# Optimization experiments

Hardware: AMD Instinct MI355X
Metric: run time of the kernel (lower is better)

## Reference

```python
import jax, jax.numpy as jnp
import numpy as np

N = 100000
H = 128
F_IN = 32
F_OUT = 16
NUM_GRAPHS = 64
NEG_SLOPE = 0.2


def setup_inputs() -> dict:
    key = jax.random.key(0)
    ks = jax.random.split(key, 16)
    inp = {
        'x': jax.random.normal(ks[0], (N, F_IN), dtype=jnp.float32),
        'edge_index': jax.random.randint(ks[1], (2, 1000000), 0, N, dtype=jnp.int32),
        'subgraph_edge_index': jax.random.randint(ks[2], (2, 1000000), 0, N, dtype=jnp.int32),
        'node_subnode_index': jax.random.randint(ks[3], (2, 200000), 0, N, dtype=jnp.int32),
        'subnode_node_index': jax.random.randint(ks[4], (2, 200000), 0, N, dtype=jnp.int32),
        'ground_node': jnp.arange(40000, dtype=jnp.int32),
        'subgraph_batch_index': jax.random.randint(ks[5], (60000,), 0, NUM_GRAPHS, dtype=jnp.int32),
        'batch_idx': jax.random.randint(ks[6], (40000,), 0, NUM_GRAPHS, dtype=jnp.int32),
    }
    s_in = 1.0 / np.sqrt(F_IN)
    s_h = 1.0 / np.sqrt(H)
    inp['emb_W'] = jax.random.uniform(ks[7], (F_IN, H), jnp.float32, -s_in, s_in)
    inp['emb_b'] = jax.random.uniform(ks[8], (H,), jnp.float32, -s_in, s_in)
    # 4 GATv2 layers (depth=1): lin_l, lin_r, att, bias per layer
    inp['Wl'] = jax.random.uniform(ks[9], (4, H, H), jnp.float32, -s_h, s_h)
    inp['Wr'] = jax.random.uniform(ks[10], (4, H, H), jnp.float32, -s_h, s_h)
    inp['att'] = jax.random.uniform(ks[11], (4, H), jnp.float32, -s_h, s_h)
    inp['bias'] = jax.random.uniform(ks[12], (4, H), jnp.float32, -s_h, s_h)
    inp['out_W'] = jax.random.uniform(ks[13], (H, F_OUT), jnp.float32, -s_h, s_h)
    inp['out_b'] = jax.random.uniform(ks[14], (F_OUT,), jnp.float32, -s_h, s_h)
    return inp


def _gatv2(x, ei, Wl, Wr, att, b):
    # add self loops (PyG GATv2Conv default add_self_loops=True)
    loops = jnp.broadcast_to(jnp.arange(N, dtype=ei.dtype)[None, :], (2, N))
    ei = jnp.concatenate([ei, loops], axis=1)
    src, dst = ei[0], ei[1]
    xl = x @ Wl  # source transform [N,H]
    xr = x @ Wr  # target transform [N,H]
    e = jax.nn.leaky_relu(xl[src] + xr[dst], NEG_SLOPE) @ att  # [E]
    m = jax.ops.segment_max(e, dst, num_segments=N)
    p = jnp.exp(e - m[dst])
    s = jax.ops.segment_sum(p, dst, num_segments=N)
    alpha = p / s[dst]
    out = jax.ops.segment_sum(alpha[:, None] * xl[src], dst, num_segments=N)
    return out + b


def reference(x, edge_index, subgraph_edge_index, node_subnode_index,
              subnode_node_index, ground_node, subgraph_batch_index, batch_idx,
              emb_W, emb_b, Wl, Wr, att, bias, out_W, out_b):
    h = x @ emb_W + emb_b
    eis = (edge_index, node_subnode_index, subgraph_edge_index, subnode_node_index)
    for i, ei in enumerate(eis):
        h = _gatv2(h, ei, Wl[i], Wr[i], att[i], bias[i])
    # global_add_pool over ground nodes
    pooled = jax.ops.segment_sum(h[ground_node], batch_idx, num_segments=NUM_GRAPHS)
    return pooled @ out_W + out_b
```

## Files before the change

kernel.cpp:

```cpp
#include <hip/hip_runtime.h>
#include <cstddef>


typedef __attribute__((ext_vector_type(8))) short bf16x8;
typedef __attribute__((ext_vector_type(4))) float f32x4;

#define NSH   10
#define CHUNK 8192
#define POOLP 256

__device__ __forceinline__ unsigned short f2bf(float f) {
  unsigned int u = __float_as_uint(f);
  u += 0x7fffu + ((u >> 16) & 1u);
  return (unsigned short)(u >> 16);
}
__device__ __forceinline__ unsigned short f2bf_rtz(float f) {
  return (unsigned short)(__float_as_uint(f) >> 16);
}
__device__ __forceinline__ float bf2f(short s) {
  return __uint_as_float(((unsigned int)(unsigned short)s) << 16);
}
__device__ __forceinline__ float2 unpk(unsigned int u) {
  return make_float2(__uint_as_float(u << 16),
                     __uint_as_float(u & 0xFFFF0000u));
}

__device__ __forceinline__ int lds_excl_scan(int* a, int len, int* aux, int tid)
{
  int g = (len + 255) >> 8;
  int lo = tid * g;
  int s = 0;
  for (int i = 0; i < g; ++i) { int idx = lo + i; if (idx < len) s += a[idx]; }
  aux[tid] = s;
  __syncthreads();
  for (int d = 1; d < 256; d <<= 1) {
    int v = (tid >= d) ? aux[tid - d] : 0;
    __syncthreads();
    aux[tid] += v;
    __syncthreads();
  }
  int run = aux[tid] - s;
  for (int i = 0; i < g; ++i) {
    int idx = lo + i;
    if (idx < len) { int t = a[idx]; a[idx] = run; run += t; }
  }
  int total = aux[255];
  __syncthreads();
  return total;
}

__device__ __forceinline__ void resolve_item(
    int id, int t1, int t2, int t3, int t4, int n,
    const int* s0, const int* s1, const int* s2, const int* s3,
    const int* d0, const int* d1, const int* d2, const int* d3,
    int& l, int& s, int& d, bool need_src)
{
  if (id < t4) {
    const int *sp, *dp; int e;
    if      (id < t1) { l = 0; e = id;      sp = s0; dp = d0; }
    else if (id < t2) { l = 1; e = id - t1; sp = s1; dp = d1; }
    else if (id < t3) { l = 2; e = id - t2; sp = s2; dp = d2; }
    else              { l = 3; e = id - t3; sp = s3; dp = d3; }
    d = dp[e];
    s = need_src ? sp[e] : 0;
  } else {
    int k = id - t4;
    l = (k >= 3 * n) ? 3 : (k >= 2 * n) ? 2 : (k >= n) ? 1 : 0;
    s = k - l * n; d = s;
  }
}

__global__ __launch_bounds__(256) void setup_kernel(
    const float* __restrict__ Wl, const float* __restrict__ Wr,
    const float* __restrict__ embW,
    unsigned short* __restrict__ packB, unsigned short* __restrict__ packE,
    int* __restrict__ offs4, int n, int e0, int e1, int e2, int e3)
{
  int id = blockIdx.x * 256 + threadIdx.x;
  if (id < 131072) {
    int j    = id & 7;
    int lane = (id >> 3) & 63;
    int kt   = (id >> 9) & 3;
    int ct   = (id >> 11) & 15;
    int l    = id >> 15;
    int k    = kt * 32 + (lane >> 4) * 8 + j;
    int col  = ct * 16 + (lane & 15);
    float v = (ct < 8) ? Wl[(size_t)l * 16384 + k * 128 + col]
                       : Wr[(size_t)l * 16384 + k * 128 + (col - 128)];
    packB[id] = f2bf(v);
  }
  int pe = id - 131072;
  if (pe >= 0 && pe < 4096) {
    int j    = pe & 7;
    int lane = (pe >> 3) & 63;
    int ct   = pe >> 9;
    int k    = (lane >> 4) * 8 + j;
    int col  = ct * 16 + (lane & 15);
    packE[pe] = f2bf(embW[k * 128 + col]);
  }
  int q = pe - 4096;
  if (q >= 0 && q < 4) {
    int El = (q == 0) ? e0 : (q == 1) ? e1 : (q == 2) ? e2 : e3;
    offs4[(size_t)q * (n + 1) + n] = El + n;
  }
}

__global__ __launch_bounds__(256) void embed_mfma_kernel(
    const float* __restrict__ x, const unsigned short* __restrict__ packE,
    const float* __restrict__ b, unsigned short* __restrict__ hb, int n)
{
  const int wave = threadIdx.x >> 6;
  const int lane = threadIdx.x & 63;
  const int rlan = lane & 15;
  const int kgrp = lane >> 4;

  bf16x8 Bf[8];
#pragma unroll
  for (int ct = 0; ct < 8; ++ct)
    Bf[ct] = *(const bf16x8*)(packE + ((size_t)ct * 64 + lane) * 8);
  float bv[8];
#pragma unroll
  for (int ct = 0; ct < 8; ++ct) bv[ct] = b[ct * 16 + rlan];

  const float4* __restrict__ x4 = (const float4*)x;
  const int ntiles = (n + 15) / 16;
  for (int tile = blockIdx.x * 4 + wave; tile < ntiles; tile += gridDim.x * 4) {
    int r = tile * 16 + rlan;
    if (r >= n) r = n - 1;
    float4 a0 = x4[(size_t)r * 8 + kgrp * 2];
    float4 a1 = x4[(size_t)r * 8 + kgrp * 2 + 1];
    bf16x8 Af;
    Af[0] = (short)f2bf(a0.x); Af[1] = (short)f2bf(a0.y);
    Af[2] = (short)f2bf(a0.z); Af[3] = (short)f2bf(a0.w);
    Af[4] = (short)f2bf(a1.x); Af[5] = (short)f2bf(a1.y);
    Af[6] = (short)f2bf(a1.z); Af[7] = (short)f2bf(a1.w);

    f32x4 acc[8];
#pragma unroll
    for (int ct = 0; ct < 8; ++ct) {
      acc[ct] = (f32x4){0.f, 0.f, 0.f, 0.f};
      acc[ct] = __builtin_amdgcn_mfma_f32_16x16x32_bf16(Af, Bf[ct], acc[ct], 0, 0, 0);
    }
    int rowb = tile * 16 + kgrp * 4;
#pragma unroll
    for (int ct = 0; ct < 8; ++ct) {
      int col = ct * 16 + rlan;
#pragma unroll
      for (int rr = 0; rr < 4; ++rr)
        if (rowb + rr < n)
          hb[(size_t)(rowb + rr) * 128 + col] = f2bf(acc[ct][rr] + bv[ct]);
    }
  }
}

__global__ __launch_bounds__(256) void gemm_mfma_kernel(
    const unsigned short* __restrict__ hb,
    const unsigned short* __restrict__ packB,
    unsigned short* __restrict__ xlb, unsigned short* __restrict__ xrb, int n)
{
  const int wave = threadIdx.x >> 6;
  const int lane = threadIdx.x & 63;
  const int rlan = lane & 15;
  const int kgrp = lane >> 4;

  bf16x8 Bf[4][4];
#pragma unroll
  for (int ct = 0; ct < 4; ++ct)
#pragma unroll
    for (int kt = 0; kt < 4; ++kt)
      Bf[ct][kt] = *(const bf16x8*)(packB +
          ((((size_t)(wave * 4 + ct)) * 4 + kt) * 64 + lane) * 8);

  unsigned short* __restrict__ outp = (wave < 2) ? xlb : xrb;
  const int colbase = (wave & 1) * 64;

  const int ntiles = (n + 31) / 32;
  for (int tile = blockIdx.x; tile < ntiles; tile += gridDim.x) {
    const int row0 = tile * 32;
    bf16x8 Af[2][4];
#pragma unroll
    for (int rt = 0; rt < 2; ++rt) {
      int r = row0 + rt * 16 + rlan;
      if (r >= n) r = n - 1;
      const unsigned short* ap = hb + (size_t)r * 128 + kgrp * 8;
#pragma unroll
      for (int kt = 0; kt < 4; ++kt)
        Af[rt][kt] = *(const bf16x8*)(ap + kt * 32);
    }
    f32x4 acc[2][4];
#pragma unroll
    for (int rt = 0; rt < 2; ++rt)
#pragma unroll
      for (int ct = 0; ct < 4; ++ct)
        acc[rt][ct] = (f32x4){0.f, 0.f, 0.f, 0.f};
#pragma unroll
    for (int kt = 0; kt < 4; ++kt)
#pragma unroll
      for (int rt = 0; rt < 2; ++rt)
#pragma unroll
        for (int ct = 0; ct < 4; ++ct)
          acc[rt][ct] = __builtin_amdgcn_mfma_f32_16x16x32_bf16(
              Af[rt][kt], Bf[ct][kt], acc[rt][ct], 0, 0, 0);
#pragma unroll
    for (int rt = 0; rt < 2; ++rt) {
      int rowb = row0 + rt * 16 + kgrp * 4;
#pragma unroll
      for (int ct = 0; ct < 4; ++ct) {
        int col = colbase + ct * 16 + rlan;
        size_t base = (size_t)rowb * 128 + col;
#pragma unroll
        for (int r = 0; r < 4; ++r)
          if (rowb + r < n)
            outp[base + (size_t)r * 128] = f2bf_rtz(acc[rt][ct][r]);
      }
    }
  }
}

__global__ __launch_bounds__(256) void hist_kernel(
    const int* __restrict__ d0, const int* __restrict__ d1,
    const int* __restrict__ d2, const int* __restrict__ d3,
    int e0, int e1, int e2, int e3, int n, int nbk, int NB, int nitems,
    int* __restrict__ mat)
{
  __shared__ int hist[512];
  int tid = threadIdx.x, c = blockIdx.x;
  for (int i = tid; i < NB; i += 256) hist[i] = 0;
  __syncthreads();
  int t1 = e0, t2 = t1 + e1, t3 = t2 + e2, t4 = t3 + e3;
  int base = c * CHUNK;
#pragma unroll
  for (int k = 0; k < CHUNK / 256; ++k) {
    int id = base + k * 256 + tid;
    if (id < nitems) {
      int l, s, d;
      resolve_item(id, t1, t2, t3, t4, n,
                   nullptr, nullptr, nullptr, nullptr, d0, d1, d2, d3,
                   l, s, d, false);
      atomicAdd(&hist[l * nbk + (d >> NSH)], 1);
    }
  }
  __syncthreads();
  for (int i = tid; i < NB; i += 256) mat[(size_t)c * NB + i] = hist[i];
}

__global__ __launch_bounds__(256) void colscan_a_kernel(
    const int* __restrict__ mat, int* __restrict__ pfx,
    int nchunk, int NB, int* __restrict__ colsum)
{
  __shared__ int col[512];
  __shared__ int aux[256];
  int gb = blockIdx.x, tid = threadIdx.x;
  for (int i = tid; i < nchunk; i += 256) col[i] = mat[(size_t)i * NB + gb];
  __syncthreads();
  int tot = lds_excl_scan(col, nchunk, aux, tid);
  for (int i = tid; i < nchunk; i += 256) pfx[(size_t)i * NB + gb] = col[i];
  if (tid == 0) colsum[gb] = tot;
}

__global__ __launch_bounds__(256) void colscan_b_kernel(
    const int* __restrict__ colsum, int NB, int* __restrict__ colscan)
{
  __shared__ int buf[512];
  __shared__ int aux[256];
  int tid = threadIdx.x;
  for (int i = tid; i < NB; i += 256) buf[i] = colsum[i];
  __syncthreads();
  int tot = lds_excl_scan(buf, NB, aux, tid);
  for (int i = tid; i < NB; i += 256) colscan[i] = buf[i];
  if (tid == 0) colscan[NB] = tot;
}

__global__ __launch_bounds__(256) void scatter_kernel(
    const int* __restrict__ s0, const int* __restrict__ s1,
    const int* __restrict__ s2, const int* __restrict__ s3,
    const int* __restrict__ d0, const int* __restrict__ d1,
    const int* __restrict__ d2, const int* __restrict__ d3,
    int e0, int e1, int e2, int e3, int n, int nbk, int NB, int nitems,
    const int* __restrict__ mat, const int* __restrict__ pfx,
    const int* __restrict__ colscan, int* __restrict__ staging)
{
  __shared__ int lbuf[CHUNK];
  __shared__ int hist[512];
  __shared__ int cur[512];
  __shared__ int basex[512];
  __shared__ int aux[256];
  int tid = threadIdx.x, c = blockIdx.x;
  for (int i = tid; i < NB; i += 256) hist[i] = mat[(size_t)c * NB + i];
  __syncthreads();
  lds_excl_scan(hist, NB, aux, tid);
  for (int i = tid; i < NB; i += 256) {
    cur[i]   = hist[i];
    basex[i] = colscan[i] + pfx[(size_t)c * NB + i];
  }
  __syncthreads();
  int t1 = e0, t2 = t1 + e1, t3 = t2 + e2, t4 = t3 + e3;
  int base = c * CHUNK;
#pragma unroll
  for (int k = 0; k < CHUNK / 256; ++k) {
    int id = base + k * 256 + tid;
    if (id < nitems) {
      int l, s, d;
      resolve_item(id, t1, t2, t3, t4, n,
                   s0, s1, s2, s3, d0, d1, d2, d3, l, s, d, true);
      int gb = l * nbk + (d >> NSH);
      int p = atomicAdd(&cur[gb], 1);
      lbuf[p] = s | ((d & ((1 << NSH) - 1)) << 17);
    }
  }
  __syncthreads();
  int wave = tid >> 6, lane = tid & 63;
  for (int gb = wave; gb < NB; gb += 4) {
    int st = hist[gb], en = cur[gb];
    int gbase = basex[gb];
    for (int j = lane; j < en - st; j += 64)
      staging[gbase + j] = lbuf[st + j];
  }
}

__global__ __launch_bounds__(256) void finalize_kernel(
    const int* __restrict__ staging, const int* __restrict__ colscan,
    int* __restrict__ offs4, int* __restrict__ csr4, int n, int nbk,
    int cb0, int cb1, int cb2, int cb3)
{
  __shared__ int cnt[1 << NSH];
  __shared__ int pos[1 << NSH];
  __shared__ int aux[256];
  int gb = blockIdx.x, tid = threadIdx.x;
  int l = gb / nbk, b = gb % nbk;
  int beg = colscan[gb], end = colscan[gb + 1];
  int node0 = b << NSH;
  int ncount = n - node0; if (ncount > (1 << NSH)) ncount = 1 << NSH;
  int cbl = (l == 0) ? cb0 : (l == 1) ? cb1 : (l == 2) ? cb2 : cb3;

  for (int i = tid; i < (1 << NSH); i += 256) cnt[i] = 0;
  __syncthreads();
  for (int t = beg + tid; t < end; t += 256)
    atomicAdd(&cnt[staging[t] >> 17], 1);
  __syncthreads();
  lds_excl_scan(cnt, 1 << NSH, aux, tid);
  for (int i = tid; i < (1 << NSH); i += 256) {
    if (i < ncount)
      offs4[(size_t)l * (n + 1) + node0 + i] = beg + cnt[i] - cbl;
    pos[i] = cnt[i];
  }
  __syncthreads();
  for (int t = beg + tid; t < end; t += 256) {
    int e = staging[t];
    int p = atomicAdd(&pos[e >> 17], 1);
    csr4[beg + p] = e & 0x1FFFF;
  }
}

__global__ __launch_bounds__(256) void gat_dst_kernel(
    const unsigned short* __restrict__ xlb,
    const unsigned short* __restrict__ xrb,
    const int* __restrict__ offs, const int* __restrict__ csr,
    const float* __restrict__ att, const float* __restrict__ bias,
    float* __restrict__ hout_f, unsigned short* __restrict__ hout_b, int n)
{
  int wid  = (blockIdx.x * 256 + threadIdx.x) >> 6;
  int lane = threadIdx.x & 63;
  if (wid >= n) return;
  int g = lane >> 4;
  int c = lane & 15;

  uint4 xru = *(const uint4*)(xrb + (size_t)wid * 128 + c * 8);
  float2 xr0 = unpk(xru.x), xr1 = unpk(xru.y);
  float2 xr2 = unpk(xru.z), xr3 = unpk(xru.w);
  const float2* att2 = (const float2*)att + c * 4;
  float2 a0 = att2[0], a1 = att2[1], a2 = att2[2], a3 = att2[3];

  int beg = offs[wid], end = offs[wid + 1];
  float ssum = 0.f;
  float2 ac0 = {0.f, 0.f}, ac1 = {0.f, 0.f};
  float2 ac2 = {0.f, 0.f}, ac3 = {0.f, 0.f};

  uint4 xu = {0, 0, 0, 0};
  {
    int j = beg + g;
    if (j < end) {
      int s = csr[j];
      xu = *(const uint4*)(xlb + (size_t)s * 128 + c * 8);
    }
  }

  for (int j0 = beg; j0 < end; j0 += 4) {
    bool act = (j0 + g) < end;
    uint4 cu = xu;
    int jn = j0 + 4 + g;
    if (jn < end) {
      int sn = csr[jn];
      xu = *(const uint4*)(xlb + (size_t)sn * 128 + c * 8);
    }
    if (act) {
      float2 xs0 = unpk(cu.x), xs1 = unpk(cu.y);
      float2 xs2 = unpk(cu.z), xs3 = unpk(cu.w);
      float2 t0 = {xs0.x + xr0.x, xs0.y + xr0.y};
      float2 t1 = {xs1.x + xr1.x, xs1.y + xr1.y};
      float2 t2 = {xs2.x + xr2.x, xs2.y + xr2.y};
      float2 t3 = {xs3.x + xr3.x, xs3.y + xr3.y};
      t0.x = fmaxf(t0.x, 0.2f * t0.x); t0.y = fmaxf(t0.y, 0.2f * t0.y);
      t1.x = fmaxf(t1.x, 0.2f * t1.x); t1.y = fmaxf(t1.y, 0.2f * t1.y);
      t2.x = fmaxf(t2.x, 0.2f * t2.x); t2.y = fmaxf(t2.y, 0.2f * t2.y);
      t3.x = fmaxf(t3.x, 0.2f * t3.x); t3.y = fmaxf(t3.y, 0.2f * t3.y);
      float2 pp = {t0.x * a0.x, t0.y * a0.y};
      pp.x = fmaf(t1.x, a1.x, pp.x); pp.y = fmaf(t1.y, a1.y, pp.y);
      pp.x = fmaf(t2.x, a2.x, pp.x); pp.y = fmaf(t2.y, a2.y, pp.y);
      pp.x = fmaf(t3.x, a3.x, pp.x); pp.y = fmaf(t3.y, a3.y, pp.y);
      float part = pp.x + pp.y;
      part += __shfl_xor(part, 1, 64);
      part += __shfl_xor(part, 2, 64);
      part += __shfl_xor(part, 4, 64);
      part += __shfl_xor(part, 8, 64);
      float p = __expf(part);
      ssum += p;
      ac0.x = fmaf(p, xs0.x, ac0.x); ac0.y = fmaf(p, xs0.y, ac0.y);
      ac1.x = fmaf(p, xs1.x, ac1.x); ac1.y = fmaf(p, xs1.y, ac1.y);
      ac2.x = fmaf(p, xs2.x, ac2.x); ac2.y = fmaf(p, xs2.y, ac2.y);
      ac3.x = fmaf(p, xs3.x, ac3.x); ac3.y = fmaf(p, xs3.y, ac3.y);
    }
  }
  float o[8] = {ac0.x, ac0.y, ac1.x, ac1.y, ac2.x, ac2.y, ac3.x, ac3.y};
#pragma unroll
  for (int k = 0; k < 8; ++k) {
    o[k] += __shfl_xor(o[k], 16, 64);
    o[k] += __shfl_xor(o[k], 32, 64);
  }
  ssum += __shfl_xor(ssum, 16, 64);
  ssum += __shfl_xor(ssum, 32, 64);

  float inv = 1.0f / ssum;
#pragma unroll
  for (int k = 0; k < 8; ++k) o[k] = fmaf(o[k], inv, bias[c * 8 + k]);

  if (lane < 16) {
    if (hout_f) {
      float4 v0 = make_float4(o[0], o[1], o[2], o[3]);
      float4 v1 = make_float4(o[4], o[5], o[6], o[7]);
      *(float4*)(hout_f + (size_t)wid * 128 + c * 8)     = v0;
      *(float4*)(hout_f + (size_t)wid * 128 + c * 8 + 4) = v1;
    } else {
      bf16x8 ob;
#pragma unroll
      for (int k = 0; k < 8; ++k) ob[k] = (short)f2bf(o[k]);
      *(bf16x8*)(hout_b + (size_t)wid * 128 + c * 8) = ob;
    }
  }
}

__global__ __launch_bounds__(256) void pool_partial_kernel(
    const float* __restrict__ h, const int* __restrict__ gnode,
    const int* __restrict__ bidx, float* __restrict__ partial, int ng)
{
  __shared__ float acc[64 * 128];
  int tid = threadIdx.x;
  for (int t = tid; t < 64 * 128; t += 256) acc[t] = 0.f;
  __syncthreads();
  int col = tid & 127, half = tid >> 7;
  for (int nd = blockIdx.x * 2 + half; nd < ng; nd += gridDim.x * 2) {
    int row = gnode[nd];
    int g   = bidx[nd];
    atomicAdd(&acc[g * 128 + col], h[(size_t)row * 128 + col]);
  }
  __syncthreads();
  float* out = partial + (size_t)blockIdx.x * 8192;
  for (int t = tid; t < 64 * 128; t += 256) out[t] = acc[t];
}

__global__ __launch_bounds__(128) void pool_out_kernel(
    const float* __restrict__ partial, const float* __restrict__ W,
    const float* __restrict__ b, float* __restrict__ out)
{
  __shared__ float pr[128];
  int g = blockIdx.x, tid = threadIdx.x;
  float s = 0.f;
  for (int p = 0; p < POOLP; ++p) s += partial[(size_t)p * 8192 + g * 128 + tid];
  pr[tid] = s;
  __syncthreads();
  if (tid < 16) {
    float acc = b[tid];
#pragma unroll
    for (int k = 0; k < 128; ++k) acc += pr[k] * W[k * 16 + tid];
    out[g * 16 + tid] = acc;
  }
}

extern "C" void kernel_launch(void* const* d_in, const int* in_sizes, int n_in,
                              void* d_out, int out_size, void* d_ws, size_t ws_size,
                              hipStream_t stream)
{
  const float* x    = (const float*)d_in[0];
  const int* ei0    = (const int*)d_in[1];
  const int* ei_sg  = (const int*)d_in[2];
  const int* ei_ns  = (const int*)d_in[3];
  const int* ei_sn  = (const int*)d_in[4];
  const int* gnode  = (const int*)d_in[5];
  const int* bidx   = (const int*)d_in[7];
  const float* embW = (const float*)d_in[8];
  const float* embB = (const float*)d_in[9];
  const float* Wl   = (const float*)d_in[10];
  const float* Wr   = (const float*)d_in[11];
  const float* att  = (const float*)d_in[12];
  const float* bias = (const float*)d_in[13];
  const float* outW = (const float*)d_in[14];
  const float* outB = (const float*)d_in[15];

  const int n  = in_sizes[0] / 32;
  const int ng = in_sizes[5];

  const int  E_arr[4] = { in_sizes[1] / 2, in_sizes[3] / 2,
                          in_sizes[2] / 2, in_sizes[4] / 2 };
  const int* eptr[4]  = { ei0, ei_ns, ei_sg, ei_sn };
  const int E_tot  = E_arr[0] + E_arr[1] + E_arr[2] + E_arr[3];
  const int nitems = E_tot + 4 * n;
  const int nbk    = (n + (1 << NSH) - 1) >> NSH;
  const int NB     = 4 * nbk;
  const int nchunk = (nitems + CHUNK - 1) / CHUNK;
  int cb[4];
  cb[0] = 0;
  for (int i = 1; i < 4; ++i) cb[i] = cb[i - 1] + E_arr[i - 1] + n;

  char* ws = (char*)d_ws;
  size_t off = 0;
  auto alloc = [&](size_t bytes) -> void* {
    void* p = ws + off;
    off = (off + bytes + 255) & ~(size_t)255;
    return p;
  };
  float*          h      = (float*)alloc((size_t)n * 128 * sizeof(float));
  unsigned short* hb     = (unsigned short*)alloc((size_t)n * 128 * sizeof(unsigned short));
  unsigned short* xlb    = (unsigned short*)alloc((size_t)n * 128 * sizeof(unsigned short));
  unsigned short* xrb    = (unsigned short*)alloc((size_t)n * 128 * sizeof(unsigned short));
  int*            offs4  = (int*)alloc((size_t)4 * (n + 1) * sizeof(int));
  int*            mat    = (int*)alloc((size_t)nchunk * NB * sizeof(int));
  int*            pfx    = (int*)alloc((size_t)nchunk * NB * sizeof(int));
  int*            colsum = (int*)alloc((size_t)NB * sizeof(int));
  int*            colscan= (int*)alloc((size_t)(NB + 1) * sizeof(int));
  int*            staging= (int*)alloc((size_t)nitems * sizeof(int));
  int*            csr4   = (int*)alloc((size_t)nitems * sizeof(int));
  unsigned short* packB  = (unsigned short*)alloc(131072 * sizeof(unsigned short));
  unsigned short* packE  = (unsigned short*)alloc(4096 * sizeof(unsigned short));
  float*          partial= (float*)alloc((size_t)POOLP * 8192 * sizeof(float));
  (void)ws_size; (void)n_in; (void)out_size;

  const int* D[4] = { eptr[0] + E_arr[0], eptr[1] + E_arr[1],
                      eptr[2] + E_arr[2], eptr[3] + E_arr[3] };

  int setup_items = 131072 + 4096 + 4;
  setup_kernel<<<(setup_items + 255) / 256, 256, 0, stream>>>(
      Wl, Wr, embW, packB, packE, offs4, n,
      E_arr[0], E_arr[1], E_arr[2], E_arr[3]);

  const int ntile16 = (n + 15) / 16;
  embed_mfma_kernel<<<(ntile16 + 3) / 4, 256, 0, stream>>>(
      x, packE, embB, hb, n);

  hist_kernel<<<nchunk, 256, 0, stream>>>(
      D[0], D[1], D[2], D[3], E_arr[0], E_arr[1], E_arr[2], E_arr[3],
      n, nbk, NB, nitems, mat);
  colscan_a_kernel<<<NB, 256, 0, stream>>>(mat, pfx, nchunk, NB, colsum);
  colscan_b_kernel<<<1, 256, 0, stream>>>(colsum, NB, colscan);
  scatter_kernel<<<nchunk, 256, 0, stream>>>(
      eptr[0], eptr[1], eptr[2], eptr[3], D[0], D[1], D[2], D[3],
      E_arr[0], E_arr[1], E_arr[2], E_arr[3], n, nbk, NB, nitems,
      mat, pfx, colscan, staging);
  finalize_kernel<<<NB, 256, 0, stream>>>(
      staging, colscan, offs4, csr4, n, nbk, cb[0], cb[1], cb[2], cb[3]);

  const int gemm_grid = ((n + 31) / 32 + 1) / 2;
  for (int l = 0; l < 4; ++l) {
    gemm_mfma_kernel<<<gemm_grid, 256, 0, stream>>>(
        hb, packB + (size_t)l * 32768, xlb, xrb, n);
    gat_dst_kernel<<<((size_t)n * 64 + 255) / 256, 256, 0, stream>>>(
        xlb, xrb, offs4 + (size_t)l * (n + 1), csr4 + cb[l],
        att + (size_t)l * 128, bias + (size_t)l * 128,
        (l == 3) ? h : nullptr, (l < 3) ? hb : nullptr, n);
  }

  pool_partial_kernel<<<POOLP, 256, 0, stream>>>(h, gnode, bidx, partial, ng);
  pool_out_kernel<<<64, 128, 0, stream>>>(partial, outW, outB, (float*)d_out);
}
```

Baseline: 563.2 us.

## Process one destination node per 16-lane group instead of per wavefront

The GATv2 aggregation kernel now assigns each destination node to a 16-lane group rather than a full 64-lane wavefront. Each group walks its edge list serially with a one-edge prefetch, which removes the cross-group reduction and the idle lanes at the end of each node's edge list. It also folds log2(e) into the attention vector so the raw exp2 instruction can be used. In exchange there is less memory-level parallelism per node, and a wave now handles four nodes whose loops diverge when their degrees differ. The code also assumes every node has at least one edge, which self loops guarantee.

```diff
diff --git a/kernel.cpp b/kernel.cpp
--- a/kernel.cpp
+++ b/kernel.cpp
@@ -359,93 +359,76 @@
     const float* __restrict__ att, const float* __restrict__ bias,
     float* __restrict__ hout_f, unsigned short* __restrict__ hout_b, int n)
 {
-  int wid  = (blockIdx.x * 256 + threadIdx.x) >> 6;
-  int lane = threadIdx.x & 63;
+  const float LOG2E = 1.4426950408889634f;
+  int wid = (blockIdx.x * 256 + threadIdx.x) >> 4;
+  int c   = threadIdx.x & 15;
   if (wid >= n) return;
-  int g = lane >> 4;
-  int c = lane & 15;
 
   uint4 xru = *(const uint4*)(xrb + (size_t)wid * 128 + c * 8);
   float2 xr0 = unpk(xru.x), xr1 = unpk(xru.y);
   float2 xr2 = unpk(xru.z), xr3 = unpk(xru.w);
   const float2* att2 = (const float2*)att + c * 4;
   float2 a0 = att2[0], a1 = att2[1], a2 = att2[2], a3 = att2[3];
+  a0.x *= LOG2E; a0.y *= LOG2E; a1.x *= LOG2E; a1.y *= LOG2E;
+  a2.x *= LOG2E; a2.y *= LOG2E; a3.x *= LOG2E; a3.y *= LOG2E;
 
   int beg = offs[wid], end = offs[wid + 1];
   float ssum = 0.f;
   float2 ac0 = {0.f, 0.f}, ac1 = {0.f, 0.f};
   float2 ac2 = {0.f, 0.f}, ac3 = {0.f, 0.f};
 
-  uint4 xu = {0, 0, 0, 0};
-  {
-    int j = beg + g;
-    if (j < end) {
-      int s = csr[j];
-      xu = *(const uint4*)(xlb + (size_t)s * 128 + c * 8);
-    }
-  }
-
-  for (int j0 = beg; j0 < end; j0 += 4) {
-    bool act = (j0 + g) < end;
+  int s0 = csr[beg];
+  uint4 xu = *(const uint4*)(xlb + (size_t)s0 * 128 + c * 8);
+
+  for (int j = beg; j < end; ++j) {
     uint4 cu = xu;
-    int jn = j0 + 4 + g;
+    int jn = j + 1;
     if (jn < end) {
       int sn = csr[jn];
       xu = *(const uint4*)(xlb + (size_t)sn * 128 + c * 8);
     }
-    if (act) {
-      float2 xs0 = unpk(cu.x), xs1 = unpk(cu.y);
-      float2 xs2 = unpk(cu.z), xs3 = unpk(cu.w);
-      float2 t0 = {xs0.x + xr0.x, xs0.y + xr0.y};
-      float2 t1 = {xs1.x + xr1.x, xs1.y + xr1.y};
-      float2 t2 = {xs2.x + xr2.x, xs2.y + xr2.y};
-      float2 t3 = {xs3.x + xr3.x, xs3.y + xr3.y};
-      t0.x = fmaxf(t0.x, 0.2f * t0.x); t0.y = fmaxf(t0.y, 0.2f * t0.y);
-      t1.x = fmaxf(t1.x, 0.2f * t1.x); t1.y = fmaxf(t1.y, 0.2f * t1.y);
-      t2.x = fmaxf(t2.x, 0.2f * t2.x); t2.y = fmaxf(t2.y, 0.2f * t2.y);
-      t3.x = fmaxf(t3.x, 0.2f * t3.x); t3.y = fmaxf(t3.y, 0.2f * t3.y);
-      float2 pp = {t0.x * a0.x, t0.y * a0.y};
-      pp.x = fmaf(t1.x, a1.x, pp.x); pp.y = fmaf(t1.y, a1.y, pp.y);
-      pp.x = fmaf(t2.x, a2.x, pp.x); pp.y = fmaf(t2.y, a2.y, pp.y);
-      pp.x = fmaf(t3.x, a3.x, pp.x); pp.y = fmaf(t3.y, a3.y, pp.y);
-      float part = pp.x + pp.y;
-      part += __shfl_xor(part, 1, 64);
-      part += __shfl_xor(part, 2, 64);
-      part += __shfl_xor(part, 4, 64);
-      part += __shfl_xor(part, 8, 64);
-      float p = __expf(part);
-      ssum += p;
-      ac0.x = fmaf(p, xs0.x, ac0.x); ac0.y = fmaf(p, xs0.y, ac0.y);
-      ac1.x = fmaf(p, xs1.x, ac1.x); ac1.y = fmaf(p, xs1.y, ac1.y);
-      ac2.x = fmaf(p, xs2.x, ac2.x); ac2.y = fmaf(p, xs2.y, ac2.y);
-      ac3.x = fmaf(p, xs3.x, ac3.x); ac3.y = fmaf(p, xs3.y, ac3.y);
-    }
-  }
+    float2 xs0 = unpk(cu.x), xs1 = unpk(cu.y);
+    float2 xs2 = unpk(cu.z), xs3 = unpk(cu.w);
+    float2 t0 = {xs0.x + xr0.x, xs0.y + xr0.y};
+    float2 t1 = {xs1.x + xr1.x, xs1.y + xr1.y};
+    float2 t2 = {xs2.x + xr2.x, xs2.y + xr2.y};
+    float2 t3 = {xs3.x + xr3.x, xs3.y + xr3.y};
+    t0.x = fmaxf(t0.x, 0.2f * t0.x); t0.y = fmaxf(t0.y, 0.2f * t0.y);
+    t1.x = fmaxf(t1.x, 0.2f * t1.x); t1.y = fmaxf(t1.y, 0.2f * t1.y);
+    t2.x = fmaxf(t2.x, 0.2f * t2.x); t2.y = fmaxf(t2.y, 0.2f * t2.y);
+    t3.x = fmaxf(t3.x, 0.2f * t3.x); t3.y = fmaxf(t3.y, 0.2f * t3.y);
+    float2 pp = {t0.x * a0.x, t0.y * a0.y};
+    pp.x = fmaf(t1.x, a1.x, pp.x); pp.y = fmaf(t1.y, a1.y, pp.y);
+    pp.x = fmaf(t2.x, a2.x, pp.x); pp.y = fmaf(t2.y, a2.y, pp.y);
+    pp.x = fmaf(t3.x, a3.x, pp.x); pp.y = fmaf(t3.y, a3.y, pp.y);
+    float part = pp.x + pp.y;
+    part += __shfl_xor(part, 1, 64);
+    part += __shfl_xor(part, 2, 64);
+    part += __shfl_xor(part, 4, 64);
+    part += __shfl_xor(part, 8, 64);
+    float p = __builtin_amdgcn_exp2f(part);
+    ssum += p;
+    ac0.x = fmaf(p, xs0.x, ac0.x); ac0.y = fmaf(p, xs0.y, ac0.y);
+    ac1.x = fmaf(p, xs1.x, ac1.x); ac1.y = fmaf(p, xs1.y, ac1.y);
+    ac2.x = fmaf(p, xs2.x, ac2.x); ac2.y = fmaf(p, xs2.y, ac2.y);
+    ac3.x = fmaf(p, xs3.x, ac3.x); ac3.y = fmaf(p, xs3.y, ac3.y);
+  }
+
+  float inv = 1.0f / ssum;
   float o[8] = {ac0.x, ac0.y, ac1.x, ac1.y, ac2.x, ac2.y, ac3.x, ac3.y};
 #pragma unroll
-  for (int k = 0; k < 8; ++k) {
-    o[k] += __shfl_xor(o[k], 16, 64);
-    o[k] += __shfl_xor(o[k], 32, 64);
-  }
-  ssum += __shfl_xor(ssum, 16, 64);
-  ssum += __shfl_xor(ssum, 32, 64);
-
-  float inv = 1.0f / ssum;
-#pragma unroll
   for (int k = 0; k < 8; ++k) o[k] = fmaf(o[k], inv, bias[c * 8 + k]);
 
-  if (lane < 16) {
-    if (hout_f) {
-      float4 v0 = make_float4(o[0], o[1], o[2], o[3]);
-      float4 v1 = make_float4(o[4], o[5], o[6], o[7]);
-      *(float4*)(hout_f + (size_t)wid * 128 + c * 8)     = v0;
-      *(float4*)(hout_f + (size_t)wid * 128 + c * 8 + 4) = v1;
-    } else {
-      bf16x8 ob;
-#pragma unroll
-      for (int k = 0; k < 8; ++k) ob[k] = (short)f2bf(o[k]);
-      *(bf16x8*)(hout_b + (size_t)wid * 128 + c * 8) = ob;
-    }
+  if (hout_f) {
+    float4 v0 = make_float4(o[0], o[1], o[2], o[3]);
+    float4 v1 = make_float4(o[4], o[5], o[6], o[7]);
+    *(float4*)(hout_f + (size_t)wid * 128 + c * 8)     = v0;
+    *(float4*)(hout_f + (size_t)wid * 128 + c * 8 + 4) = v1;
+  } else {
+    bf16x8 ob;
+#pragma unroll
+    for (int k = 0; k < 8; ++k) ob[k] = (short)f2bf(o[k]);
+    *(bf16x8*)(hout_b + (size_t)wid * 128 + c * 8) = ob;
   }
 }
 
@@ -572,7 +555,7 @@
   for (int l = 0; l < 4; ++l) {
     gemm_mfma_kernel<<<gemm_grid, 256, 0, stream>>>(
         hb, packB + (size_t)l * 32768, xlb, xrb, n);
-    gat_dst_kernel<<<((size_t)n * 64 + 255) / 256, 256, 0, stream>>>(
+    gat_dst_kernel<<<((size_t)n * 16 + 255) / 256, 256, 0, stream>>>(
         xlb, xrb, offs4 + (size_t)l * (n + 1), csr4 + cb[l],
         att + (size_t)l * 128, bias + (size_t)l * 128,
         (l == 3) ? h : nullptr, (l < 3) ? hb : nullptr, n);
```

Result: faster. 512.0 us (-9.1%).
